# Kernel optimization log

Hardware: AMD Instinct MI355X
Metric: run time of the kernel (lower is better)

Reference implementation:

```python
import jax, jax.numpy as jnp
import numpy as np

V, E, H, W, S, T, B = 10000, 256, 512, 256, 512, 128, 64


def setup_inputs() -> dict:
    key = jax.random.key(0)
    ks = jax.random.split(key, 17)
    def rn(k, shape, s=0.08):
        return jax.random.normal(k, shape, jnp.float32) * s
    return {
        "tokens": jax.random.randint(ks[0], (B, S), 0, V),
        "dec_h0": jax.random.normal(ks[1], (B, H), jnp.float32),
        "emb_table": rn(ks[2], (V, E), 1.0),
        "enc_Wih": rn(ks[3], (4 * H, E)),
        "enc_Whh": rn(ks[4], (4 * H, H)),
        "enc_bih": rn(ks[5], (4 * H,)),
        "enc_bhh": rn(ks[6], (4 * H,)),
        "dec_Wih": rn(ks[7], (4 * H, E)),
        "dec_Whh": rn(ks[8], (4 * H, H)),
        "dec_bih": rn(ks[9], (4 * H,)),
        "dec_bhh": rn(ks[10], (4 * H,)),
        "W1_w": rn(ks[11], (W, H)),
        "W1_b": rn(ks[12], (W,)),
        "W2_w": rn(ks[13], (W, H)),
        "W2_b": rn(ks[14], (W,)),
        "vt_w": rn(ks[15], (1, W)),
        "vt_b": rn(ks[16], (1,)),
    }


def _lstm_cell(x, h, c, Wih, Whh, bih, bhh):
    # PyTorch gate order: input, forget, cell(g), output
    gates = x @ Wih.T + h @ Whh.T + bih + bhh
    i, f, g, o = jnp.split(gates, 4, axis=-1)
    c = jax.nn.sigmoid(f) * c + jax.nn.sigmoid(i) * jnp.tanh(g)
    h = jax.nn.sigmoid(o) * jnp.tanh(c)
    return h, c


def reference(tokens, dec_h0, emb_table, enc_Wih, enc_Whh, enc_bih, enc_bhh,
              dec_Wih, dec_Whh, dec_bih, dec_bhh, W1_w, W1_b, W2_w, W2_b,
              vt_w, vt_b):
    emb = emb_table[tokens]                       # [B,S,E]
    x_sbe = jnp.swapaxes(emb, 0, 1)               # [S,B,E] time-major
    bsz = tokens.shape[0]
    h0 = jnp.zeros((bsz, enc_Whh.shape[1]), emb.dtype)

    def enc_step(carry, x):
        h, c = carry
        h, c = _lstm_cell(x, h, c, enc_Wih, enc_Whh, enc_bih, enc_bhh)
        return (h, c), h

    _, enc_states = jax.lax.scan(enc_step, (h0, h0), x_sbe)   # [S,B,H]

    # W1(encoder_states) is constant across decoder steps -> hoist it
    blend1 = enc_states @ W1_w.T + W1_b            # [S,B,W]
    c0 = enc_states[-1]                            # original uses last enc state as cell init
    dec_in = jnp.zeros((bsz, emb_table.shape[1]), emb.dtype)  # never updated in original

    def dec_step(carry, _):
        h, c = carry
        h, c = _lstm_cell(dec_in, h, c, dec_Wih, dec_Whh, dec_bih, dec_bhh)
        blend2 = h @ W2_w.T + W2_b                 # [B,W]
        u = (jnp.tanh(blend1 + blend2[None]) @ vt_w.T)[..., 0] + vt_b[0]  # [S,B]
        logp = jax.nn.log_softmax(u.T, axis=1)     # [B,S], softmax over seq positions
        return (h, c), logp

    _, probs = jax.lax.scan(dec_step, (dec_h0, c0), None, length=T)  # [T,B,S]
    return jnp.swapaxes(probs, 0, 1)               # [B,T,S]
```

## Files before the change

### kernel.cpp

```cpp
#include <hip/hip_runtime.h>
#include <hip/hip_bf16.h>
#include <cstdint>
#include <cstddef>

typedef __bf16 bf16_t;
typedef __bf16 bf16x8 __attribute__((ext_vector_type(8)));
typedef float  f32x4  __attribute__((ext_vector_type(4)));

#define NB 64
#define NS 512
#define NTD 128
#define NE 256
#define NH 512
#define NG 2048
#define NW 256

#define HSTEP_DW 16384u
#define FPAD 16

__device__ __forceinline__ float sigm_f(float x) { return 1.f / (1.f + __expf(-x)); }
__device__ __forceinline__ float tanh_f(float x) {
  float e = __expf(2.f * x);
  return 1.f - 2.f / (e + 1.f);
}
__device__ __forceinline__ float bits2f(uint32_t b16) {
  uint32_t u = b16 << 16;
  return __builtin_bit_cast(float, u);
}
__device__ __forceinline__ uint32_t aload(const uint32_t* p) {
  return __hip_atomic_load(p, __ATOMIC_RELAXED, __HIP_MEMORY_SCOPE_AGENT);
}
__device__ __forceinline__ uint64_t aload64(const uint64_t* p) {
  return __hip_atomic_load(p, __ATOMIC_RELAXED, __HIP_MEMORY_SCOPE_AGENT);
}
__device__ __forceinline__ void astore(uint32_t* p, uint32_t v) {
  __hip_atomic_store(p, v, __ATOMIC_RELAXED, __HIP_MEMORY_SCOPE_AGENT);
}
__device__ __forceinline__ void astoref(float* p, float v) {
  __hip_atomic_store((uint32_t*)p, __builtin_bit_cast(uint32_t, v),
                     __ATOMIC_RELAXED, __HIP_MEMORY_SCOPE_AGENT);
}
__device__ __forceinline__ float aloadf(const float* p) {
  return __builtin_bit_cast(float, aload((const uint32_t*)p));
}
__device__ __forceinline__ void drain_vm() {
  asm volatile("s_waitcnt vmcnt(0)" ::: "memory");
}
__device__ __forceinline__ float xpick(uint2 v, int r) {
  uint32_t d = (r < 2) ? v.x : v.y;
  return bits2f((r & 1) ? (d >> 16) : (d & 0xffffu));
}

__global__ __launch_bounds__(256) void pack_b(const float* __restrict__ src,
                                              bf16_t* __restrict__ dst,
                                              int N, int K) {
  int idx = blockIdx.x * 256 + threadIdx.x;
  if (idx >= N * K) return;
  int n = idx / K, k = idx - n * K;
  int lane = (((k & 31) >> 3) << 4) | (n & 15);
  size_t o = ((((size_t)(n >> 4) * (K >> 5)) + (k >> 5)) * 64 + lane) * 8 + (k & 7);
  dst[o] = (bf16_t)src[idx];
}

__global__ __launch_bounds__(256) void gather_emb(const int* __restrict__ tokens,
                                                  const float* __restrict__ table,
                                                  bf16_t* __restrict__ embfrag) {
  int idx = blockIdx.x * 256 + threadIdx.x;
  int row = idx >> 5, e0 = (idx & 31) << 3;
  int b = row & 63, s = row >> 6;
  int tok = tokens[b * NS + s];
  const float4* p = (const float4*)(table + (size_t)tok * NE + e0);
  float4 v0 = p[0], v1 = p[1];
  bf16x8 v;
  v[0] = (bf16_t)v0.x; v[1] = (bf16_t)v0.y; v[2] = (bf16_t)v0.z; v[3] = (bf16_t)v0.w;
  v[4] = (bf16_t)v1.x; v[5] = (bf16_t)v1.y; v[6] = (bf16_t)v1.z; v[7] = (bf16_t)v1.w;
  int mt = row >> 4;
  int ks = e0 >> 5;
  int lane = (b & 15) | (((e0 >> 3) & 3) << 4);
  *(bf16x8*)(embfrag + ((size_t)(mt * 8 + ks) * 64 + lane) * 8) = v;
}

__global__ __launch_bounds__(256) void pack_h0(const float* __restrict__ src,
                                               uint32_t* __restrict__ dst) {
  int idx = blockIdx.x * 256 + threadIdx.x;
  int b = idx >> 8, jp = idx & 255;
  int j = jp * 2;
  float lo = src[(size_t)b * NH + j], hi = src[(size_t)b * NH + j + 1];
  uint16_t l16 = __builtin_bit_cast(uint16_t, (bf16_t)lo);
  uint16_t h16 = __builtin_bit_cast(uint16_t, (bf16_t)hi);
  int bg = b >> 4, bl = b & 15, ks = j >> 5;
  int lane = bl | (((j >> 3) & 3) << 4);
  dst[((size_t)bg * 16 + ks) * 256 + lane * 4 + ((j >> 1) & 3)] =
      (uint32_t)l16 | ((uint32_t)h16 << 16);
}

__global__ __launch_bounds__(256) void gemm_xih(const bf16_t* __restrict__ A,
                                                const bf16_t* __restrict__ Bp,
                                                bf16_t* __restrict__ out,
                                                const float* __restrict__ b1,
                                                const float* __restrict__ b2) {
  const int KS = 8, MT = 16;
  int lane = threadIdx.x & 63, w = threadIdx.x >> 6;
  int nt = blockIdx.x * 4 + w;
  int mt0 = blockIdx.y * MT;
  bf16x8 bfr[KS];
  const bf16_t* bp = Bp + ((size_t)nt * KS * 64 + lane) * 8;
#pragma unroll
  for (int ks = 0; ks < KS; ++ks) bfr[ks] = *(const bf16x8*)(bp + (size_t)ks * 512);
  int n = (nt << 4) + (lane & 15);
  float bs = b1[n] + b2[n];
  int g = nt >> 5, sl = (nt & 31) >> 1, ct = nt & 1;
  for (int m = 0; m < MT; ++m) {
    int mt = mt0 + m;
    const bf16_t* ap = A + (size_t)mt * (KS * 512) + lane * 8;
    f32x4 acc = {0.f, 0.f, 0.f, 0.f};
#pragma unroll
    for (int ks = 0; ks < KS; ++ks)
      acc = __builtin_amdgcn_mfma_f32_16x16x32_bf16(
          *(const bf16x8*)(ap + (size_t)ks * 512), bfr[ks], acc, 0, 0, 0);
    ushort4 hv;
    hv.x = __builtin_bit_cast(uint16_t, (bf16_t)(acc[0] + bs));
    hv.y = __builtin_bit_cast(uint16_t, (bf16_t)(acc[1] + bs));
    hv.z = __builtin_bit_cast(uint16_t, (bf16_t)(acc[2] + bs));
    hv.w = __builtin_bit_cast(uint16_t, (bf16_t)(acc[3] + bs));
    *(ushort4*)(out + ((((size_t)mt * 16 + sl) * 2 + ct) * 4 + g) * 256 + lane * 4) = hv;
  }
}

__global__ __launch_bounds__(256) void enc_chain(
    const bf16_t* __restrict__ Wp, const bf16_t* __restrict__ xih2,
    const bf16_t* __restrict__ W1p, const float* __restrict__ W1_b,
    uint32_t* __restrict__ hfrag, uint32_t* __restrict__ flags,
    bf16_t* __restrict__ blend1) {
  __shared__ bf16_t wlds[8 * 8192];
  __shared__ bf16_t wb[8192];
  int tid = threadIdx.x, lane = tid & 63, wid = tid >> 6;
  int bg = blockIdx.x >> 4, slice = blockIdx.x & 15;

  for (int l = 0; l < 8; ++l) {
    int g = l >> 1, p = l & 1;
    const bf16_t* s = Wp + (size_t)(g * 32 + slice * 2 + p) * 8192;
    for (int i = tid; i < 1024; i += 256)
      *(bf16x8*)(wlds + l * 8192 + (size_t)i * 8) = *(const bf16x8*)(s + (size_t)i * 8);
  }
  {
    const bf16_t* s = W1p + (size_t)slice * 8192;
    for (int i = tid; i < 1024; i += 256)
      *(bf16x8*)(wb + (size_t)i * 8) = *(const bf16x8*)(s + (size_t)i * 8);
  }
  __syncthreads();
  if (wid == 3) return;

  const uint64_t* hq = (const uint64_t*)hfrag;
  uint32_t* fbase = flags + bg * 32 * FPAD;
  int c = lane & 15, grp = lane >> 4;

  if (wid < 2) {
    int ct = wid;
    int j = slice * 32 + ct * 16 + c;
    int sub = (j >> 3) & 3, dw = (j >> 1) & 3;
    uint32_t* myflag = fbase + (slice * 2 + ct) * FPAD;
    float cst[4] = {0.f, 0.f, 0.f, 0.f};
    const bf16_t* wb0 = wlds + (size_t)(0 * 2 + ct) * 8192;
    const bf16_t* wb1 = wlds + (size_t)(1 * 2 + ct) * 8192;
    const bf16_t* wb2 = wlds + (size_t)(2 * 2 + ct) * 8192;
    const bf16_t* wb3 = wlds + (size_t)(3 * 2 + ct) * 8192;
    for (int t = 0; t < NS; ++t) {
      const uint32_t* xb = (const uint32_t*)xih2 +
          ((((size_t)t * 4 + bg) * 16 + slice) * 2 + ct) * 512 + lane * 2;
      uint2 xg0 = *(const uint2*)(xb);
      uint2 xg1 = *(const uint2*)(xb + 128);
      uint2 xg2 = *(const uint2*)(xb + 256);
      uint2 xg3 = *(const uint2*)(xb + 384);
      if (t > 0) {
        uint32_t tgt = (uint32_t)t; bool ok;
        do {
          uint32_t f = tgt;
          if (lane < 32) f = aload(fbase + lane * FPAD);
          ok = __all(f >= tgt);
        } while (!ok);
      }
      const uint64_t* hb = hq + ((size_t)t * 4 + bg) * 2048 + lane * 2;
      uint64_t aq[16][2];
#pragma unroll
      for (int ks = 0; ks < 16; ++ks) {
        aq[ks][0] = aload64(hb + (size_t)ks * 128);
        aq[ks][1] = aload64(hb + (size_t)ks * 128 + 1);
      }
      f32x4 a0 = {0.f,0.f,0.f,0.f}, a1 = a0, a2 = a0, a3 = a0;
#pragma unroll
      for (int ks = 0; ks < 16; ++ks) {
        union { uint64_t q[2]; bf16x8 v; } u;
        u.q[0] = aq[ks][0]; u.q[1] = aq[ks][1];
        int o = ks * 512 + lane * 8;
        a0 = __builtin_amdgcn_mfma_f32_16x16x32_bf16(u.v, *(const bf16x8*)(wb0 + o), a0, 0, 0, 0);
        a1 = __builtin_amdgcn_mfma_f32_16x16x32_bf16(u.v, *(const bf16x8*)(wb1 + o), a1, 0, 0, 0);
        a2 = __builtin_amdgcn_mfma_f32_16x16x32_bf16(u.v, *(const bf16x8*)(wb2 + o), a2, 0, 0, 0);
        a3 = __builtin_amdgcn_mfma_f32_16x16x32_bf16(u.v, *(const bf16x8*)(wb3 + o), a3, 0, 0, 0);
      }
      uint32_t hsb = ((uint32_t)(t + 1) * 4 + (uint32_t)bg) * 4096 + slice * 256;
#pragma unroll
      for (int r = 0; r < 4; ++r) {
        float pi = a0[r] + xpick(xg0, r), pf = a1[r] + xpick(xg1, r);
        float pg = a2[r] + xpick(xg2, r), po = a3[r] + xpick(xg3, r);
        float iG = sigm_f(pi), fG = sigm_f(pf), gG = tanh_f(pg), oG = sigm_f(po);
        cst[r] = fG * cst[r] + iG * gG;
        float h = oG * tanh_f(cst[r]);
        uint16_t hv = __builtin_bit_cast(uint16_t, (bf16_t)h);
        uint32_t other = (uint32_t)__shfl_xor((int)(uint32_t)hv, 1, 64);
        if (!(lane & 1)) {
          uint32_t dword = (uint32_t)hv | (other << 16);
          astore(hfrag + (size_t)hsb + (((grp * 4 + r) | (sub << 4)) * 4 + dw), dword);
        }
      }
      drain_vm();
      if (lane == 0) astore(myflag, (uint32_t)(t + 1));
    }
  } else {
    float bb = W1_b[slice * 16 + c];
    for (int t = 1; t <= NS; ++t) {
      uint32_t tgt = (uint32_t)t; bool ok;
      do {
        uint32_t f = tgt;
        if (lane < 32) f = aload(fbase + lane * FPAD);
        ok = __all(f >= tgt);
      } while (!ok);
      const uint64_t* hb = hq + ((size_t)t * 4 + bg) * 2048 + lane * 2;
      f32x4 acc = {0.f, 0.f, 0.f, 0.f};
#pragma unroll
      for (int ks = 0; ks < 16; ++ks) {
        union { uint64_t q[2]; bf16x8 v; } u;
        u.q[0] = aload64(hb + (size_t)ks * 128);
        u.q[1] = aload64(hb + (size_t)ks * 128 + 1);
        acc = __builtin_amdgcn_mfma_f32_16x16x32_bf16(
            u.v, *(const bf16x8*)(wb + ks * 512 + lane * 8), acc, 0, 0, 0);
      }
      size_t row = (size_t)(t - 1) * 64 + bg * 16 + grp * 4;
#pragma unroll
      for (int r = 0; r < 4; ++r)
        blend1[(row + r) * 256 + slice * 16 + c] = (bf16_t)(acc[r] + bb);
    }
  }
}

__global__ __launch_bounds__(256) void dec_attn(
    const bf16_t* __restrict__ Wp, const float* __restrict__ bih,
    const float* __restrict__ bhh, const bf16_t* __restrict__ W2p,
    const float* __restrict__ W2_b, uint32_t* __restrict__ hfrag,
    const uint32_t* __restrict__ c0frag, uint32_t* __restrict__ dflags,
    uint32_t* __restrict__ bl2f, const bf16_t* __restrict__ blend1,
    float* __restrict__ blend2, const float* __restrict__ vt_w,
    float* __restrict__ out) {
  union SM {
    struct { bf16_t wlds[8 * 8192]; bf16_t wb[8192]; } c;
    struct { float vt[272], b2[272], u[512], red[8]; } a;
  };
  __shared__ SM sm;
  int tid = threadIdx.x, lane = tid & 63, wid = tid >> 6;

  if (blockIdx.x < 64) {
    int bg = blockIdx.x >> 4, slice = blockIdx.x & 15;
    for (int l = 0; l < 8; ++l) {
      int g = l >> 1, p = l & 1;
      const bf16_t* s = Wp + (size_t)(g * 32 + slice * 2 + p) * 8192;
      for (int i = tid; i < 1024; i += 256)
        *(bf16x8*)(sm.c.wlds + l * 8192 + (size_t)i * 8) = *(const bf16x8*)(s + (size_t)i * 8);
    }
    {
      const bf16_t* s = W2p + (size_t)slice * 8192;
      for (int i = tid; i < 1024; i += 256)
        *(bf16x8*)(sm.c.wb + (size_t)i * 8) = *(const bf16x8*)(s + (size_t)i * 8);
    }
    __syncthreads();
    if (wid == 3) return;

    const uint64_t* hq = (const uint64_t*)hfrag;
    uint32_t* fbase = dflags + bg * 32 * FPAD;
    int c = lane & 15, grp = lane >> 6 ? 0 : lane >> 4;
    grp = lane >> 4;

    if (wid < 2) {
      int ct = wid;
      int j = slice * 32 + ct * 16 + c;
      int sub = (j >> 3) & 3, dw = (j >> 1) & 3, half = j & 1;
      uint32_t* myflag = fbase + (slice * 2 + ct) * FPAD;
      float bs0 = bih[0 * NH + j] + bhh[0 * NH + j];
      float bs1 = bih[1 * NH + j] + bhh[1 * NH + j];
      float bs2 = bih[2 * NH + j] + bhh[2 * NH + j];
      float bs3 = bih[3 * NH + j] + bhh[3 * NH + j];
      float cst[4];
#pragma unroll
      for (int r = 0; r < 4; ++r) {
        uint32_t d = c0frag[(size_t)(bg * 16 + slice) * 256 +
                            (((grp * 4 + r) | (sub << 4)) * 4 + dw)];
        cst[r] = half ? bits2f(d >> 16) : bits2f(d & 0xffffu);
      }
      const bf16_t* wb0 = sm.c.wlds + (size_t)(0 * 2 + ct) * 8192;
      const bf16_t* wb1 = sm.c.wlds + (size_t)(1 * 2 + ct) * 8192;
      const bf16_t* wb2 = sm.c.wlds + (size_t)(2 * 2 + ct) * 8192;
      const bf16_t* wb3 = sm.c.wlds + (size_t)(3 * 2 + ct) * 8192;
      for (int t = 0; t < NTD; ++t) {
        if (t > 0) {
          uint32_t tgt = (uint32_t)t; bool ok;
          do {
            uint32_t f = tgt;
            if (lane < 32) f = aload(fbase + lane * FPAD);
            ok = __all(f >= tgt);
          } while (!ok);
        }
        const uint64_t* hb = hq + ((size_t)t * 4 + bg) * 2048 + lane * 2;
        uint64_t aq[16][2];
#pragma unroll
        for (int ks = 0; ks < 16; ++ks) {
          aq[ks][0] = aload64(hb + (size_t)ks * 128);
          aq[ks][1] = aload64(hb + (size_t)ks * 128 + 1);
        }
        f32x4 a0 = {0.f,0.f,0.f,0.f}, a1 = a0, a2 = a0, a3 = a0;
#pragma unroll
        for (int ks = 0; ks < 16; ++ks) {
          union { uint64_t q[2]; bf16x8 v; } u;
          u.q[0] = aq[ks][0]; u.q[1] = aq[ks][1];
          int o = ks * 512 + lane * 8;
          a0 = __builtin_amdgcn_mfma_f32_16x16x32_bf16(u.v, *(const bf16x8*)(wb0 + o), a0, 0, 0, 0);
          a1 = __builtin_amdgcn_mfma_f32_16x16x32_bf16(u.v, *(const bf16x8*)(wb1 + o), a1, 0, 0, 0);
          a2 = __builtin_amdgcn_mfma_f32_16x16x32_bf16(u.v, *(const bf16x8*)(wb2 + o), a2, 0, 0, 0);
          a3 = __builtin_amdgcn_mfma_f32_16x16x32_bf16(u.v, *(const bf16x8*)(wb3 + o), a3, 0, 0, 0);
        }
        uint32_t hsb = ((uint32_t)(t + 1) * 4 + (uint32_t)bg) * 4096 + slice * 256;
#pragma unroll
        for (int r = 0; r < 4; ++r) {
          float iG = sigm_f(a0[r] + bs0), fG = sigm_f(a1[r] + bs1);
          float gG = tanh_f(a2[r] + bs2), oG = sigm_f(a3[r] + bs3);
          cst[r] = fG * cst[r] + iG * gG;
          float h = oG * tanh_f(cst[r]);
          uint16_t hv = __builtin_bit_cast(uint16_t, (bf16_t)h);
          uint32_t other = (uint32_t)__shfl_xor((int)(uint32_t)hv, 1, 64);
          if (!(lane & 1)) {
            uint32_t dword = (uint32_t)hv | (other << 16);
            astore(hfrag + (size_t)hsb + (((grp * 4 + r) | (sub << 4)) * 4 + dw), dword);
          }
        }
        drain_vm();
        if (lane == 0) astore(myflag, (uint32_t)(t + 1));
      }
    } else {
      float bb = W2_b[slice * 16 + c];
      uint32_t* myb = bl2f + (bg * 16 + slice) * FPAD;
      for (int t = 1; t <= NTD; ++t) {
        uint32_t tgt = (uint32_t)t; bool ok;
        do {
          uint32_t f = tgt;
          if (lane < 32) f = aload(fbase + lane * FPAD);
          ok = __all(f >= tgt);
        } while (!ok);
        const uint64_t* hb = hq + ((size_t)t * 4 + bg) * 2048 + lane * 2;
        f32x4 acc = {0.f, 0.f, 0.f, 0.f};
#pragma unroll
        for (int ks = 0; ks < 16; ++ks) {
          union { uint64_t q[2]; bf16x8 v; } u;
          u.q[0] = aload64(hb + (size_t)ks * 128);
          u.q[1] = aload64(hb + (size_t)ks * 128 + 1);
          acc = __builtin_amdgcn_mfma_f32_16x16x32_bf16(
              u.v, *(const bf16x8*)(sm.c.wb + ks * 512 + lane * 8), acc, 0, 0, 0);
        }
        size_t row = (size_t)(t - 1) * 64 + bg * 16 + grp * 4;
#pragma unroll
        for (int r = 0; r < 4; ++r)
          astoref(blend2 + (row + r) * 256 + slice * 16 + c, acc[r] + bb);
        drain_vm();
        if (lane == 0) astore(myb, (uint32_t)t);
      }
    }
  } else {
    int w = blockIdx.x - 64;
    for (int k = w; k < NTD * NB; k += 192) {
      int t = k >> 6, b = k & 63, bgb = b >> 4;
      if (wid == 0) {
        uint32_t tgt = (uint32_t)(t + 1); bool ok;
        do {
          uint32_t f = tgt;
          if (lane < 16) f = aload(bl2f + (bgb * 16 + lane) * FPAD);
          ok = __all(f >= tgt);
          if (!ok) __builtin_amdgcn_s_sleep(16);
        } while (!ok);
      }
      __syncthreads();
      {
        int ww = tid;
        int pi = ww + ((ww >> 6) << 2);
        sm.a.vt[pi] = vt_w[ww];
        sm.a.b2[pi] = aloadf(blend2 + (size_t)(t * 64 + b) * NW + ww);
      }
      __syncthreads();
      int wgrp = lane >> 4, sgrp = lane & 15;
      int base = wgrp * 68;
      for (int it = 0; it < 8; ++it) {
        int s = it * 64 + wid * 16 + sgrp;
        const bf16_t* row = blend1 + ((size_t)s * NB + b) * NW + wgrp * 64;
        float val = 0.f;
#pragma unroll
        for (int c8 = 0; c8 < 8; ++c8) {
          bf16x8 v = *(const bf16x8*)(row + c8 * 8);
#pragma unroll
          for (int jx = 0; jx < 8; ++jx) {
            int wi = base + c8 * 8 + jx;
            val += sm.a.vt[wi] * tanh_f((float)v[jx] + sm.a.b2[wi]);
          }
        }
        val += __shfl_xor(val, 16, 64);
        val += __shfl_xor(val, 32, 64);
        if (wgrp == 0) sm.a.u[it * 64 + wid * 16 + sgrp] = val;
      }
      __syncthreads();
      float a = sm.a.u[tid], bb2 = sm.a.u[tid + 256];
      float m = fmaxf(a, bb2);
#pragma unroll
      for (int o = 1; o < 64; o <<= 1) m = fmaxf(m, __shfl_xor(m, o, 64));
      if (lane == 0) sm.a.red[wid] = m;
      __syncthreads();
      m = fmaxf(fmaxf(sm.a.red[0], sm.a.red[1]), fmaxf(sm.a.red[2], sm.a.red[3]));
      float e = __expf(a - m) + __expf(bb2 - m);
#pragma unroll
      for (int o = 1; o < 64; o <<= 1) e += __shfl_xor(e, o, 64);
      if (lane == 0) sm.a.red[4 + wid] = e;
      __syncthreads();
      float lz = m + logf(sm.a.red[4] + sm.a.red[5] + sm.a.red[6] + sm.a.red[7]);
      size_t ob = ((size_t)b * NTD + t) * NS;
      out[ob + tid] = a - lz;
      out[ob + tid + 256] = bb2 - lz;
      __syncthreads();
    }
  }
}

extern "C" void kernel_launch(void* const* d_in, const int* in_sizes, int n_in,
                              void* d_out, int out_size, void* d_ws, size_t ws_size,
                              hipStream_t stream) {
  const int*   tokens    = (const int*)d_in[0];
  const float* dec_h0    = (const float*)d_in[1];
  const float* emb_table = (const float*)d_in[2];
  const float* enc_Wih   = (const float*)d_in[3];
  const float* enc_Whh   = (const float*)d_in[4];
  const float* enc_bih   = (const float*)d_in[5];
  const float* enc_bhh   = (const float*)d_in[6];
  const float* dec_Whh   = (const float*)d_in[8];
  const float* dec_bih   = (const float*)d_in[9];
  const float* dec_bhh   = (const float*)d_in[10];
  const float* W1_w      = (const float*)d_in[11];
  const float* W1_b      = (const float*)d_in[12];
  const float* W2_w      = (const float*)d_in[13];
  const float* W2_b      = (const float*)d_in[14];
  const float* vt_w      = (const float*)d_in[15];
  float* out = (float*)d_out;

  char* w = (char*)d_ws;
  size_t off = 0;
  auto alloc = [&](size_t bytes) {
    size_t o = off;
    off += (bytes + 255) & ~(size_t)255;
    return o;
  };
  bf16_t* embfrag = (bf16_t*)(w + alloc((size_t)NS * NB * NE * 2));
  bf16_t* xih2    = (bf16_t*)(w + alloc((size_t)NS * NB * NG * 2));
  uint32_t* enc_hf = (uint32_t*)(w + alloc((size_t)(NS + 1) * HSTEP_DW * 4));
  uint32_t* dec_hf = (uint32_t*)(w + alloc((size_t)(NTD + 1) * HSTEP_DW * 4));
  bf16_t* blend1  = (bf16_t*)(w + alloc((size_t)NS * NB * NW * 2));
  float*  blend2  = (float*)(w + alloc((size_t)NTD * NB * NW * 4));
  bf16_t* pWih    = (bf16_t*)(w + alloc((size_t)NG * NE * 2));
  bf16_t* pWhhE   = (bf16_t*)(w + alloc((size_t)NG * NH * 2));
  bf16_t* pWhhD   = (bf16_t*)(w + alloc((size_t)NG * NH * 2));
  bf16_t* pW1     = (bf16_t*)(w + alloc((size_t)NW * NH * 2));
  bf16_t* pW2     = (bf16_t*)(w + alloc((size_t)NW * NH * 2));
  uint32_t* flags = (uint32_t*)(w + alloc(5120 * 4));
  (void)ws_size; (void)in_sizes; (void)n_in; (void)out_size;

  hipMemsetAsync(flags, 0, 5120 * 4, stream);
  hipMemsetAsync(enc_hf, 0, HSTEP_DW * 4, stream);

  pack_b<<<(NG * NE) / 256, 256, 0, stream>>>(enc_Wih, pWih, NG, NE);
  pack_b<<<(NG * NH) / 256, 256, 0, stream>>>(enc_Whh, pWhhE, NG, NH);
  pack_b<<<(NG * NH) / 256, 256, 0, stream>>>(dec_Whh, pWhhD, NG, NH);
  pack_b<<<(NW * NH) / 256, 256, 0, stream>>>(W1_w, pW1, NW, NH);
  pack_b<<<(NW * NH) / 256, 256, 0, stream>>>(W2_w, pW2, NW, NH);

  gather_emb<<<(NS * NB * (NE / 8)) / 256, 256, 0, stream>>>(tokens, emb_table, embfrag);
  pack_h0<<<64, 256, 0, stream>>>(dec_h0, dec_hf);

  gemm_xih<<<dim3(128 / 4, 2048 / 16), 256, 0, stream>>>(
      embfrag, pWih, xih2, enc_bih, enc_bhh);

  enc_chain<<<64, 256, 0, stream>>>(pWhhE, xih2, pW1, W1_b, enc_hf, flags, blend1);

  dec_attn<<<256, 256, 0, stream>>>(pWhhD, dec_bih, dec_bhh, pW2, W2_b, dec_hf,
                                    enc_hf + (size_t)NS * HSTEP_DW,
                                    flags + 2048, flags + 4096,
                                    blend1, blend2, vt_w, out);
}
```

Baseline: 3.285 ms.

## Replace flag-based step synchronization with sentinel-valued data polling

```diff
diff --git a/kernel.cpp b/kernel.cpp
--- a/kernel.cpp
+++ b/kernel.cpp
@@ -16,7 +16,7 @@
 #define NW 256
 
 #define HSTEP_DW 16384u
-#define FPAD 16
+#define SENT32 0xFFFFFFFFu
 
 __device__ __forceinline__ float sigm_f(float x) { return 1.f / (1.f + __expf(-x)); }
 __device__ __forceinline__ float tanh_f(float x) {
@@ -40,15 +40,12 @@
   __hip_atomic_store((uint32_t*)p, __builtin_bit_cast(uint32_t, v),
                      __ATOMIC_RELAXED, __HIP_MEMORY_SCOPE_AGENT);
 }
-__device__ __forceinline__ float aloadf(const float* p) {
-  return __builtin_bit_cast(float, aload((const uint32_t*)p));
-}
-__device__ __forceinline__ void drain_vm() {
-  asm volatile("s_waitcnt vmcnt(0)" ::: "memory");
-}
 __device__ __forceinline__ float xpick(uint2 v, int r) {
   uint32_t d = (r < 2) ? v.x : v.y;
   return bits2f((r & 1) ? (d >> 16) : (d & 0xffffu));
+}
+__device__ __forceinline__ bool q_bad(uint64_t q) {
+  return ((uint32_t)q == SENT32) | ((uint32_t)(q >> 32) == SENT32);
 }
 
 __global__ __launch_bounds__(256) void pack_b(const float* __restrict__ src,
@@ -127,11 +124,26 @@
   }
 }
 
+__device__ __forceinline__ void poll_h(const uint64_t* hb, uint64_t aq[16][2]) {
+  for (;;) {
+    bool bad = false;
+#pragma unroll
+    for (int ks = 0; ks < 16; ++ks) {
+      aq[ks][0] = aload64(hb + (size_t)ks * 128);
+      aq[ks][1] = aload64(hb + (size_t)ks * 128 + 1);
+    }
+#pragma unroll
+    for (int ks = 0; ks < 16; ++ks)
+      bad |= q_bad(aq[ks][0]) | q_bad(aq[ks][1]);
+    if (!__any(bad)) return;
+    __builtin_amdgcn_s_sleep(1);
+  }
+}
+
 __global__ __launch_bounds__(256) void enc_chain(
     const bf16_t* __restrict__ Wp, const bf16_t* __restrict__ xih2,
     const bf16_t* __restrict__ W1p, const float* __restrict__ W1_b,
-    uint32_t* __restrict__ hfrag, uint32_t* __restrict__ flags,
-    bf16_t* __restrict__ blend1) {
+    uint32_t* __restrict__ hfrag, bf16_t* __restrict__ blend1) {
   __shared__ bf16_t wlds[8 * 8192];
   __shared__ bf16_t wb[8192];
   int tid = threadIdx.x, lane = tid & 63, wid = tid >> 6;
@@ -152,14 +164,12 @@
   if (wid == 3) return;
 
   const uint64_t* hq = (const uint64_t*)hfrag;
-  uint32_t* fbase = flags + bg * 32 * FPAD;
   int c = lane & 15, grp = lane >> 4;
 
   if (wid < 2) {
     int ct = wid;
     int j = slice * 32 + ct * 16 + c;
     int sub = (j >> 3) & 3, dw = (j >> 1) & 3;
-    uint32_t* myflag = fbase + (slice * 2 + ct) * FPAD;
     float cst[4] = {0.f, 0.f, 0.f, 0.f};
     const bf16_t* wb0 = wlds + (size_t)(0 * 2 + ct) * 8192;
     const bf16_t* wb1 = wlds + (size_t)(1 * 2 + ct) * 8192;
@@ -172,21 +182,9 @@
       uint2 xg1 = *(const uint2*)(xb + 128);
       uint2 xg2 = *(const uint2*)(xb + 256);
       uint2 xg3 = *(const uint2*)(xb + 384);
-      if (t > 0) {
-        uint32_t tgt = (uint32_t)t; bool ok;
-        do {
-          uint32_t f = tgt;
-          if (lane < 32) f = aload(fbase + lane * FPAD);
-          ok = __all(f >= tgt);
-        } while (!ok);
-      }
       const uint64_t* hb = hq + ((size_t)t * 4 + bg) * 2048 + lane * 2;
       uint64_t aq[16][2];
-#pragma unroll
-      for (int ks = 0; ks < 16; ++ks) {
-        aq[ks][0] = aload64(hb + (size_t)ks * 128);
-        aq[ks][1] = aload64(hb + (size_t)ks * 128 + 1);
-      }
+      poll_h(hb, aq);
       f32x4 a0 = {0.f,0.f,0.f,0.f}, a1 = a0, a2 = a0, a3 = a0;
 #pragma unroll
       for (int ks = 0; ks < 16; ++ks) {
@@ -213,25 +211,18 @@
           astore(hfrag + (size_t)hsb + (((grp * 4 + r) | (sub << 4)) * 4 + dw), dword);
         }
       }
-      drain_vm();
-      if (lane == 0) astore(myflag, (uint32_t)(t + 1));
     }
   } else {
     float bb = W1_b[slice * 16 + c];
     for (int t = 1; t <= NS; ++t) {
-      uint32_t tgt = (uint32_t)t; bool ok;
-      do {
-        uint32_t f = tgt;
-        if (lane < 32) f = aload(fbase + lane * FPAD);
-        ok = __all(f >= tgt);
-      } while (!ok);
       const uint64_t* hb = hq + ((size_t)t * 4 + bg) * 2048 + lane * 2;
+      uint64_t aq[16][2];
+      poll_h(hb, aq);
       f32x4 acc = {0.f, 0.f, 0.f, 0.f};
 #pragma unroll
       for (int ks = 0; ks < 16; ++ks) {
         union { uint64_t q[2]; bf16x8 v; } u;
-        u.q[0] = aload64(hb + (size_t)ks * 128);
-        u.q[1] = aload64(hb + (size_t)ks * 128 + 1);
+        u.q[0] = aq[ks][0]; u.q[1] = aq[ks][1];
         acc = __builtin_amdgcn_mfma_f32_16x16x32_bf16(
             u.v, *(const bf16x8*)(wb + ks * 512 + lane * 8), acc, 0, 0, 0);
       }
@@ -247,8 +238,7 @@
     const bf16_t* __restrict__ Wp, const float* __restrict__ bih,
     const float* __restrict__ bhh, const bf16_t* __restrict__ W2p,
     const float* __restrict__ W2_b, uint32_t* __restrict__ hfrag,
-    const uint32_t* __restrict__ c0frag, uint32_t* __restrict__ dflags,
-    uint32_t* __restrict__ bl2f, const bf16_t* __restrict__ blend1,
+    const uint32_t* __restrict__ c0frag, const bf16_t* __restrict__ blend1,
     float* __restrict__ blend2, const float* __restrict__ vt_w,
     float* __restrict__ out) {
   union SM {
@@ -275,15 +265,12 @@
     if (wid == 3) return;
 
     const uint64_t* hq = (const uint64_t*)hfrag;
-    uint32_t* fbase = dflags + bg * 32 * FPAD;
-    int c = lane & 15, grp = lane >> 6 ? 0 : lane >> 4;
-    grp = lane >> 4;
+    int c = lane & 15, grp = lane >> 4;
 
     if (wid < 2) {
       int ct = wid;
       int j = slice * 32 + ct * 16 + c;
       int sub = (j >> 3) & 3, dw = (j >> 1) & 3, half = j & 1;
-      uint32_t* myflag = fbase + (slice * 2 + ct) * FPAD;
       float bs0 = bih[0 * NH + j] + bhh[0 * NH + j];
       float bs1 = bih[1 * NH + j] + bhh[1 * NH + j];
       float bs2 = bih[2 * NH + j] + bhh[2 * NH + j];
@@ -300,21 +287,9 @@
       const bf16_t* wb2 = sm.c.wlds + (size_t)(2 * 2 + ct) * 8192;
       const bf16_t* wb3 = sm.c.wlds + (size_t)(3 * 2 + ct) * 8192;
       for (int t = 0; t < NTD; ++t) {
-        if (t > 0) {
-          uint32_t tgt = (uint32_t)t; bool ok;
-          do {
-            uint32_t f = tgt;
-            if (lane < 32) f = aload(fbase + lane * FPAD);
-            ok = __all(f >= tgt);
-          } while (!ok);
-        }
         const uint64_t* hb = hq + ((size_t)t * 4 + bg) * 2048 + lane * 2;
         uint64_t aq[16][2];
-#pragma unroll
-        for (int ks = 0; ks < 16; ++ks) {
-          aq[ks][0] = aload64(hb + (size_t)ks * 128);
-          aq[ks][1] = aload64(hb + (size_t)ks * 128 + 1);
-        }
+        poll_h(hb, aq);
         f32x4 a0 = {0.f,0.f,0.f,0.f}, a1 = a0, a2 = a0, a3 = a0;
 #pragma unroll
         for (int ks = 0; ks < 16; ++ks) {
@@ -340,26 +315,18 @@
             astore(hfrag + (size_t)hsb + (((grp * 4 + r) | (sub << 4)) * 4 + dw), dword);
           }
         }
-        drain_vm();
-        if (lane == 0) astore(myflag, (uint32_t)(t + 1));
       }
     } else {
       float bb = W2_b[slice * 16 + c];
-      uint32_t* myb = bl2f + (bg * 16 + slice) * FPAD;
       for (int t = 1; t <= NTD; ++t) {
-        uint32_t tgt = (uint32_t)t; bool ok;
-        do {
-          uint32_t f = tgt;
-          if (lane < 32) f = aload(fbase + lane * FPAD);
-          ok = __all(f >= tgt);
-        } while (!ok);
         const uint64_t* hb = hq + ((size_t)t * 4 + bg) * 2048 + lane * 2;
+        uint64_t aq[16][2];
+        poll_h(hb, aq);
         f32x4 acc = {0.f, 0.f, 0.f, 0.f};
 #pragma unroll
         for (int ks = 0; ks < 16; ++ks) {
           union { uint64_t q[2]; bf16x8 v; } u;
-          u.q[0] = aload64(hb + (size_t)ks * 128);
-          u.q[1] = aload64(hb + (size_t)ks * 128 + 1);
+          u.q[0] = aq[ks][0]; u.q[1] = aq[ks][1];
           acc = __builtin_amdgcn_mfma_f32_16x16x32_bf16(
               u.v, *(const bf16x8*)(sm.c.wb + ks * 512 + lane * 8), acc, 0, 0, 0);
         }
@@ -367,29 +334,19 @@
 #pragma unroll
         for (int r = 0; r < 4; ++r)
           astoref(blend2 + (row + r) * 256 + slice * 16 + c, acc[r] + bb);
-        drain_vm();
-        if (lane == 0) astore(myb, (uint32_t)t);
       }
     }
   } else {
     int w = blockIdx.x - 64;
     for (int k = w; k < NTD * NB; k += 192) {
-      int t = k >> 6, b = k & 63, bgb = b >> 4;
-      if (wid == 0) {
-        uint32_t tgt = (uint32_t)(t + 1); bool ok;
-        do {
-          uint32_t f = tgt;
-          if (lane < 16) f = aload(bl2f + (bgb * 16 + lane) * FPAD);
-          ok = __all(f >= tgt);
-          if (!ok) __builtin_amdgcn_s_sleep(16);
-        } while (!ok);
-      }
-      __syncthreads();
+      int t = k >> 6, b = k & 63;
       {
-        int ww = tid;
-        int pi = ww + ((ww >> 6) << 2);
-        sm.a.vt[pi] = vt_w[ww];
-        sm.a.b2[pi] = aloadf(blend2 + (size_t)(t * 64 + b) * NW + ww);
+        const uint32_t* b2p = (const uint32_t*)blend2 + (size_t)(t * 64 + b) * NW + tid;
+        uint32_t v = aload(b2p);
+        while (v == SENT32) { __builtin_amdgcn_s_sleep(2); v = aload(b2p); }
+        int pi = tid + ((tid >> 6) << 2);
+        sm.a.b2[pi] = __builtin_bit_cast(float, v);
+        sm.a.vt[pi] = vt_w[tid];
       }
       __syncthreads();
       int wgrp = lane >> 4, sgrp = lane & 15;
@@ -471,11 +428,12 @@
   bf16_t* pWhhD   = (bf16_t*)(w + alloc((size_t)NG * NH * 2));
   bf16_t* pW1     = (bf16_t*)(w + alloc((size_t)NW * NH * 2));
   bf16_t* pW2     = (bf16_t*)(w + alloc((size_t)NW * NH * 2));
-  uint32_t* flags = (uint32_t*)(w + alloc(5120 * 4));
   (void)ws_size; (void)in_sizes; (void)n_in; (void)out_size;
 
-  hipMemsetAsync(flags, 0, 5120 * 4, stream);
-  hipMemsetAsync(enc_hf, 0, HSTEP_DW * 4, stream);
+  hipMemsetAsync(enc_hf, 0xFF, (size_t)(NS + 1) * HSTEP_DW * 4, stream);
+  hipMemsetAsync(enc_hf, 0x00, HSTEP_DW * 4, stream);
+  hipMemsetAsync(dec_hf + HSTEP_DW, 0xFF, (size_t)NTD * HSTEP_DW * 4, stream);
+  hipMemsetAsync(blend2, 0xFF, (size_t)NTD * NB * NW * 4, stream);
 
   pack_b<<<(NG * NE) / 256, 256, 0, stream>>>(enc_Wih, pWih, NG, NE);
   pack_b<<<(NG * NH) / 256, 256, 0, stream>>>(enc_Whh, pWhhE, NG, NH);
@@ -489,10 +447,9 @@
   gemm_xih<<<dim3(128 / 4, 2048 / 16), 256, 0, stream>>>(
       embfrag, pWih, xih2, enc_bih, enc_bhh);
 
-  enc_chain<<<64, 256, 0, stream>>>(pWhhE, xih2, pW1, W1_b, enc_hf, flags, blend1);
+  enc_chain<<<64, 256, 0, stream>>>(pWhhE, xih2, pW1, W1_b, enc_hf, blend1);
 
   dec_attn<<<256, 256, 0, stream>>>(pWhhD, dec_bih, dec_bhh, pW2, W2_b, dec_hf,
                                     enc_hf + (size_t)NS * HSTEP_DW,
-                                    flags + 2048, flags + 4096,
                                     blend1, blend2, vt_w, out);
 }
```

Measured after the change: 3.885 ms. 1.18x slower.
